# Kernel tuning notes

Hardware: AMD Instinct MI355X
Metric: run time of the kernel (lower is better)

## Reference

```python
import jax, jax.numpy as jnp
import numpy as np

N_U = 16          # |U| unary predicates
N_B = 8           # |B| binary predicates
N_NODES = 500000
N_EDGES = 2000000

# Parsed clause structure: (literal column indices, literal signs).
# Unary clauses over the |U|=16 unary predicate columns.
U_CLAUSES = [
    (np.array([0, 1]), np.array([-1.0, 1.0])),
    (np.array([2, 3]), np.array([-1.0, 1.0])),
    (np.array([4, 5, 6]), np.array([-1.0, 1.0, 1.0])),
]
# Binary clauses over the joined [2|U|+|B|]=40 space: x-copy offset 0, y-copy offset 16, binary offset 32.
B_CLAUSES = [
    (np.array([0, 16, 32]), np.array([-1.0, -1.0, 1.0])),
    (np.array([1, 17, 33]), np.array([-1.0, 1.0, 1.0])),
]


def knowledge_enhancer(x, clauses, weights):
    """KENN KnowledgeEnhancer with GodelBoostConormApprox boost.
    For each clause: delta = w * softmax(signed literals) * signs, scattered back.
    """
    delta = jnp.zeros_like(x)
    for (idx, sign), w in zip(clauses, weights):
        s = jnp.asarray(sign, x.dtype)
        v = x[:, idx] * s                      # [rows, clause_len]
        d = w * jax.nn.softmax(v, axis=-1) * s
        delta = delta.at[:, idx].add(d)
    return delta


def setup_inputs() -> dict:
    key = jax.random.key(0)
    k1, k2, k3, k4 = jax.random.split(key, 4)
    unary = jax.random.normal(k1, (N_NODES, N_U), jnp.float32)
    binary = jax.random.normal(k2, (N_EDGES, N_B), jnp.float32)
    edge_index = jax.random.randint(k3, (2, N_EDGES), 0, N_NODES)
    edge_weight = jax.random.uniform(k4, (N_EDGES,), jnp.float32)
    unary_clause_weights = jnp.full((len(U_CLAUSES),), 0.5, jnp.float32)
    binary_clause_weights = jnp.full((len(B_CLAUSES),), 0.5, jnp.float32)
    return {
        "unary": unary,
        "binary": binary,
        "edge_index": edge_index,
        "edge_weight": edge_weight,
        "unary_clause_weights": unary_clause_weights,
        "binary_clause_weights": binary_clause_weights,
    }


def reference(unary, binary, edge_index, edge_weight, unary_clause_weights, binary_clause_weights):
    i1, i2 = edge_index[0], edge_index[1]
    # unary KE
    u = unary + knowledge_enhancer(unary, U_CLAUSES, unary_clause_weights)
    # Join: gather both endpoints and concat with binary features -> [E, 2|U|+|B|]
    joined = jnp.concatenate([u[i1], u[i2], binary], axis=1)
    # binary KE, per-edge weighted
    d = knowledge_enhancer(joined, B_CLAUSES, binary_clause_weights) * edge_weight[:, None]
    ux = d[:, :N_U]
    uy = d[:, N_U:2 * N_U]
    db = d[:, 2 * N_U:]
    # GroupBy: indexed assignment (last-write semantics, matching torch tensor[index] = val)
    delta_up = jnp.zeros_like(u).at[i1].set(ux) + jnp.zeros_like(u).at[i2].set(uy)
    # activation is identity (default)
    return (u + delta_up, binary + db)
```

## Files before the change

### kernel.cpp

```cpp
#include <hip/hip_runtime.h>
#include <hip/hip_bf16.h>

typedef unsigned long long u64;

__device__ __forceinline__ float bf2f(unsigned short u) {
    union { unsigned int i; float f; } x; x.i = ((unsigned int)u) << 16; return x.f;
}
__device__ __forceinline__ unsigned short f2bf(float f) {
    union { float f; unsigned int i; } x; x.f = f;
    unsigned int r = x.i + 0x7fffu + ((x.i >> 16) & 1u);
    return (unsigned short)(r >> 16);
}

__device__ __forceinline__ bool detect_bf16(const void* unary) {
    const uint4* p = (const uint4*)unary;
    int plaus = 0;
    #pragma unroll
    for (int i = 0; i < 8; ++i) {
        uint4 v = p[i];
        unsigned int w[4] = {v.x, v.y, v.z, v.w};
        #pragma unroll
        for (int j = 0; j < 4; ++j) {
            int ex = (int)((w[j] >> 7) & 0xffu);
            if (ex >= 114 && ex <= 129) ++plaus;
        }
    }
    return plaus >= 16;
}

__device__ __forceinline__ float ldf(const void* p, size_t i, bool bf) {
    return bf ? bf2f(((const unsigned short*)p)[i]) : ((const float*)p)[i];
}


__global__ void f_init(const void* __restrict__ unary,
                       const void* __restrict__ wu,
                       unsigned int* __restrict__ u01,
                       u64* __restrict__ lastA,
                       u64* __restrict__ lastB,
                       unsigned int* __restrict__ shA,
                       unsigned int* __restrict__ shB,
                       int n_nodes)
{
    int n = blockIdx.x * blockDim.x + threadIdx.x;
    if (n >= n_nodes) return;
    bool bf = detect_bf16(unary);
    float x0 = ldf(unary, (size_t)n * 16 + 0, bf);
    float x1 = ldf(unary, (size_t)n * 16 + 1, bf);
    float w0 = ldf(wu, 0, bf);
    float t0 = __expf(-x0), t1 = __expf(x1), inv = w0 / (t0 + t1);
    x0 -= t0 * inv; x1 += t1 * inv;
    u01[n] = (unsigned int)f2bf(x0) | ((unsigned int)f2bf(x1) << 16);
    lastA[n] = 0ull;
    lastB[n] = 0ull;
    shA[n] = 0u;
    shB[n] = 0u;
}

__global__ void f_edge(const void* __restrict__ unary,
                       const void* __restrict__ binary,
                       const int*  __restrict__ ei,
                       const void* __restrict__ ew,
                       const void* __restrict__ wb,
                       const unsigned int* __restrict__ u01,
                       void* __restrict__ out0,
                       u64* __restrict__ lastA,
                       u64* __restrict__ lastB,
                       unsigned int* __restrict__ shA,
                       unsigned int* __restrict__ shB,
                       int n_nodes, int n_edges)
{
    int gid = blockIdx.x * blockDim.x + threadIdx.x;
    if (gid >= n_edges) return;
    int e = n_edges - 1 - gid;
    bool bf = detect_bf16(unary);
    size_t esz = bf ? 2u : 4u;
    char* out1 = (char*)out0 + (size_t)n_nodes * 16u * esz;

    int i1 = ei[e];
    int i2 = ei[e + n_edges];

    unsigned int pa = u01[i1];
    unsigned int pb = u01[i2];
    float a0 = bf2f((unsigned short)(pa & 0xffffu));
    float a1 = bf2f((unsigned short)(pa >> 16));
    float b0 = bf2f((unsigned short)(pb & 0xffffu));
    float b1 = bf2f((unsigned short)(pb >> 16));

    float c0 = ldf(binary, (size_t)e * 8 + 0, bf);
    float c1 = ldf(binary, (size_t)e * 8 + 1, bf);
    float w   = ldf(ew, e, bf);
    float wb0 = ldf(wb, 0, bf);
    float wb1 = ldf(wb, 1, bf);

    float tA0 = __expf(-a0), tA1 = __expf(-b0), tA2 = __expf(c0);
    float invA = w * wb0 / (tA0 + tA1 + tA2);
    float ux0 = -tA0 * invA, uy0 = -tA1 * invA, db0 = tA2 * invA;
    float tB0 = __expf(-a1), tB1 = __expf(b1), tB2 = __expf(c1);
    float invB = w * wb1 / (tB0 + tB1 + tB2);
    float ux1 = -tB0 * invB, uy1 = tB1 * invB, db1 = tB2 * invB;

    if (bf) {
        unsigned short el[8];
        *(uint4*)el = *(const uint4*)((const char*)binary + (size_t)e * 16);
        el[0] = f2bf(c0 + db0);
        el[1] = f2bf(c1 + db1);
        *(uint4*)(out1 + (size_t)e * 16) = *(uint4*)el;
    } else {
        const float* src = (const float*)binary + (size_t)e * 8;
        float r[8];
        *(uint4*)&r[0] = *(const uint4*)&src[0];
        *(uint4*)&r[4] = *(const uint4*)&src[4];
        r[0] = c0 + db0;
        r[1] = c1 + db1;
        float* dst = (float*)(out1 + (size_t)e * 32);
        *(uint4*)&dst[0] = *(uint4*)&r[0];
        *(uint4*)&dst[4] = *(uint4*)&r[4];
    }

    unsigned int key = (unsigned int)(e + 1);
    unsigned int qa = (unsigned int)f2bf(ux0) | ((unsigned int)f2bf(ux1) << 16);
    unsigned int qb = (unsigned int)f2bf(uy0) | ((unsigned int)f2bf(uy1) << 16);
    if (shA[i1] < key) {
        shA[i1] = key;
        atomicMax(&lastA[i1], ((u64)key << 32) | qa);
    }
    if (shB[i2] < key) {
        shB[i2] = key;
        atomicMax(&lastB[i2], ((u64)key << 32) | qb);
    }
}

__global__ void f_fin(const void* __restrict__ unary,
                      const void* __restrict__ wu,
                      const u64* __restrict__ lastA,
                      const u64* __restrict__ lastB,
                      void* __restrict__ out0,
                      int n_nodes)
{
    int n = blockIdx.x * blockDim.x + threadIdx.x;
    if (n >= n_nodes) return;
    bool bf = detect_bf16(unary);

    float x[16];
    if (bf) {
        const unsigned short* src = (const unsigned short*)unary + (size_t)n * 16;
        unsigned short el[16];
        *(uint4*)&el[0] = *(const uint4*)&src[0];
        *(uint4*)&el[8] = *(const uint4*)&src[8];
        #pragma unroll
        for (int i = 0; i < 16; ++i) x[i] = bf2f(el[i]);
    } else {
        const float* src = (const float*)unary + (size_t)n * 16;
        #pragma unroll
        for (int i = 0; i < 16; i += 4) *(uint4*)&x[i] = *(const uint4*)&src[i];
    }

    float w0 = ldf(wu, 0, bf), w1 = ldf(wu, 1, bf), w2 = ldf(wu, 2, bf);
    { float t0 = __expf(-x[0]), t1 = __expf(x[1]), inv = w0 / (t0 + t1);
      x[0] -= t0 * inv; x[1] += t1 * inv; }
    { float t0 = __expf(-x[2]), t1 = __expf(x[3]), inv = w1 / (t0 + t1);
      x[2] -= t0 * inv; x[3] += t1 * inv; }
    { float t0 = __expf(-x[4]), t1 = __expf(x[5]), t2 = __expf(x[6]);
      float inv = w2 / (t0 + t1 + t2);
      x[4] -= t0 * inv; x[5] += t1 * inv; x[6] += t2 * inv; }

    u64 sa = lastA[n], sb = lastB[n];
    if (sa) {
        x[0] += bf2f((unsigned short)(sa & 0xffffu));
        x[1] += bf2f((unsigned short)((sa >> 16) & 0xffffu));
    }
    if (sb) {
        x[0] += bf2f((unsigned short)(sb & 0xffffu));
        x[1] += bf2f((unsigned short)((sb >> 16) & 0xffffu));
    }

    if (bf) {
        unsigned short el[16];
        #pragma unroll
        for (int i = 0; i < 16; ++i) el[i] = f2bf(x[i]);
        uint4* dst = (uint4*)((char*)out0 + (size_t)n * 32);
        dst[0] = *(uint4*)&el[0];
        dst[1] = *(uint4*)&el[8];
    } else {
        float* dst = (float*)((char*)out0 + (size_t)n * 64);
        #pragma unroll
        for (int i = 0; i < 16; i += 4) *(uint4*)&dst[i] = *(uint4*)&x[i];
    }
}


__global__ void m_edge(const void* __restrict__ unary,
                       const void* __restrict__ binary,
                       const int*  __restrict__ ei,
                       const void* __restrict__ ew,
                       const void* __restrict__ wb,
                       const unsigned int* __restrict__ u01,
                       void* __restrict__ out0,
                       u64* __restrict__ lastA,
                       u64* __restrict__ lastB,
                       int n_nodes, int n_edges)
{
    int gid = blockIdx.x * blockDim.x + threadIdx.x;
    if (gid >= n_edges) return;
    int e = n_edges - 1 - gid;
    bool bf = detect_bf16(unary);
    size_t esz = bf ? 2u : 4u;
    char* out1 = (char*)out0 + (size_t)n_nodes * 16u * esz;

    int i1 = ei[e];
    int i2 = ei[e + n_edges];

    unsigned int pa = u01[i1];
    unsigned int pb = u01[i2];
    float a0 = bf2f((unsigned short)(pa & 0xffffu));
    float a1 = bf2f((unsigned short)(pa >> 16));
    float b0 = bf2f((unsigned short)(pb & 0xffffu));
    float b1 = bf2f((unsigned short)(pb >> 16));

    float c0 = ldf(binary, (size_t)e * 8 + 0, bf);
    float c1 = ldf(binary, (size_t)e * 8 + 1, bf);
    float w   = ldf(ew, e, bf);
    float wb0 = ldf(wb, 0, bf);
    float wb1 = ldf(wb, 1, bf);

    float tA0 = __expf(-a0), tA1 = __expf(-b0), tA2 = __expf(c0);
    float invA = w * wb0 / (tA0 + tA1 + tA2);
    float ux0 = -tA0 * invA, uy0 = -tA1 * invA, db0 = tA2 * invA;
    float tB0 = __expf(-a1), tB1 = __expf(b1), tB2 = __expf(c1);
    float invB = w * wb1 / (tB0 + tB1 + tB2);
    float ux1 = -tB0 * invB, uy1 = tB1 * invB, db1 = tB2 * invB;

    if (bf) {
        unsigned short el[8];
        *(uint4*)el = *(const uint4*)((const char*)binary + (size_t)e * 16);
        el[0] = f2bf(c0 + db0);
        el[1] = f2bf(c1 + db1);
        *(uint4*)(out1 + (size_t)e * 16) = *(uint4*)el;
    } else {
        const float* src = (const float*)binary + (size_t)e * 8;
        float r[8];
        *(uint4*)&r[0] = *(const uint4*)&src[0];
        *(uint4*)&r[4] = *(const uint4*)&src[4];
        r[0] = c0 + db0;
        r[1] = c1 + db1;
        float* dst = (float*)(out1 + (size_t)e * 32);
        *(uint4*)&dst[0] = *(uint4*)&r[0];
        *(uint4*)&dst[4] = *(uint4*)&r[4];
    }

    unsigned int key = (unsigned int)(e + 1);
    unsigned int qa = (unsigned int)f2bf(ux0) | ((unsigned int)f2bf(ux1) << 16);
    unsigned int qb = (unsigned int)f2bf(uy0) | ((unsigned int)f2bf(uy1) << 16);
    if ((unsigned int)(lastA[i1] >> 32) < key)
        atomicMax(&lastA[i1], ((u64)key << 32) | qa);
    if ((unsigned int)(lastB[i2] >> 32) < key)
        atomicMax(&lastB[i2], ((u64)key << 32) | qb);
}


__global__ void k_init(const void* __restrict__ unary, void* __restrict__ out0,
                       int n_nodes)
{
    int n = blockIdx.x * blockDim.x + threadIdx.x;
    if (n >= n_nodes) return;
    bool bf = detect_bf16(unary);
    size_t rs = bf ? 32u : 64u;
    u64* s = (u64*)((char*)out0 + (size_t)n * rs);
    s[0] = 0ull; s[1] = 0ull;
}

__global__ void k_edge(const void* __restrict__ unary,
                       const void* __restrict__ binary,
                       const int*  __restrict__ ei,
                       const void* __restrict__ ew,
                       const void* __restrict__ wu,
                       const void* __restrict__ wb,
                       void* __restrict__ out0,
                       int n_nodes, int n_edges)
{
    int e = blockIdx.x * blockDim.x + threadIdx.x;
    if (e >= n_edges) return;
    bool bf = detect_bf16(unary);
    size_t esz = bf ? 2u : 4u;
    size_t rs  = 16u * esz;
    char* out1 = (char*)out0 + (size_t)n_nodes * rs;

    int i1 = ei[e];
    int i2 = ei[e + n_edges];

    float w0 = ldf(wu, 0, bf);
    float a0 = ldf(unary, (size_t)i1 * 16 + 0, bf);
    float a1 = ldf(unary, (size_t)i1 * 16 + 1, bf);
    { float t0 = __expf(-a0), t1 = __expf(a1), inv = w0 / (t0 + t1);
      a0 -= t0 * inv; a1 += t1 * inv; }
    float b0 = ldf(unary, (size_t)i2 * 16 + 0, bf);
    float b1 = ldf(unary, (size_t)i2 * 16 + 1, bf);
    { float t0 = __expf(-b0), t1 = __expf(b1), inv = w0 / (t0 + t1);
      b0 -= t0 * inv; b1 += t1 * inv; }

    float c0 = ldf(binary, (size_t)e * 8 + 0, bf);
    float c1 = ldf(binary, (size_t)e * 8 + 1, bf);
    float w   = ldf(ew, e, bf);
    float wb0 = ldf(wb, 0, bf);
    float wb1 = ldf(wb, 1, bf);

    float tA0 = __expf(-a0), tA1 = __expf(-b0), tA2 = __expf(c0);
    float invA = w * wb0 / (tA0 + tA1 + tA2);
    float ux0 = -tA0 * invA, uy0 = -tA1 * invA, db0 = tA2 * invA;
    float tB0 = __expf(-a1), tB1 = __expf(b1), tB2 = __expf(c1);
    float invB = w * wb1 / (tB0 + tB1 + tB2);
    float ux1 = -tB0 * invB, uy1 = tB1 * invB, db1 = tB2 * invB;

    if (bf) {
        unsigned short el[8];
        *(uint4*)el = *(const uint4*)((const char*)binary + (size_t)e * 16);
        el[0] = f2bf(c0 + db0);
        el[1] = f2bf(c1 + db1);
        *(uint4*)(out1 + (size_t)e * 16) = *(uint4*)el;
    } else {
        const float* src = (const float*)binary + (size_t)e * 8;
        float r[8];
        *(uint4*)&r[0] = *(const uint4*)&src[0];
        *(uint4*)&r[4] = *(const uint4*)&src[4];
        r[0] = c0 + db0;
        r[1] = c1 + db1;
        float* dst = (float*)(out1 + (size_t)e * 32);
        *(uint4*)&dst[0] = *(uint4*)&r[0];
        *(uint4*)&dst[4] = *(uint4*)&r[4];
    }

    unsigned int pa = (unsigned int)f2bf(ux0) | ((unsigned int)f2bf(ux1) << 16);
    unsigned int pb = (unsigned int)f2bf(uy0) | ((unsigned int)f2bf(uy1) << 16);
    u64 ka = ((u64)(unsigned int)(e + 1) << 32) | pa;
    u64 kb = ((u64)(unsigned int)(e + 1) << 32) | pb;
    atomicMax((u64*)((char*)out0 + (size_t)i1 * rs),     ka);
    atomicMax((u64*)((char*)out0 + (size_t)i2 * rs + 8), kb);
}

__global__ void k_fin(const void* __restrict__ unary,
                      const void* __restrict__ wu,
                      void* __restrict__ out0,
                      int n_nodes)
{
    int n = blockIdx.x * blockDim.x + threadIdx.x;
    if (n >= n_nodes) return;
    bool bf = detect_bf16(unary);
    size_t rs = bf ? 32u : 64u;
    char* row = (char*)out0 + (size_t)n * rs;

    u64 sa = ((const u64*)row)[0];
    u64 sb = ((const u64*)row)[1];

    float x[16];
    if (bf) {
        const unsigned short* src = (const unsigned short*)unary + (size_t)n * 16;
        unsigned short el[16];
        *(uint4*)&el[0] = *(const uint4*)&src[0];
        *(uint4*)&el[8] = *(const uint4*)&src[8];
        #pragma unroll
        for (int i = 0; i < 16; ++i) x[i] = bf2f(el[i]);
    } else {
        const float* src = (const float*)unary + (size_t)n * 16;
        #pragma unroll
        for (int i = 0; i < 16; i += 4) *(uint4*)&x[i] = *(const uint4*)&src[i];
    }

    float w0 = ldf(wu, 0, bf), w1 = ldf(wu, 1, bf), w2 = ldf(wu, 2, bf);
    { float t0 = __expf(-x[0]), t1 = __expf(x[1]), inv = w0 / (t0 + t1);
      x[0] -= t0 * inv; x[1] += t1 * inv; }
    { float t0 = __expf(-x[2]), t1 = __expf(x[3]), inv = w1 / (t0 + t1);
      x[2] -= t0 * inv; x[3] += t1 * inv; }
    { float t0 = __expf(-x[4]), t1 = __expf(x[5]), t2 = __expf(x[6]);
      float inv = w2 / (t0 + t1 + t2);
      x[4] -= t0 * inv; x[5] += t1 * inv; x[6] += t2 * inv; }

    if (sa) {
        x[0] += bf2f((unsigned short)(sa & 0xffffu));
        x[1] += bf2f((unsigned short)((sa >> 16) & 0xffffu));
    }
    if (sb) {
        x[0] += bf2f((unsigned short)(sb & 0xffffu));
        x[1] += bf2f((unsigned short)((sb >> 16) & 0xffffu));
    }

    if (bf) {
        unsigned short el[16];
        #pragma unroll
        for (int i = 0; i < 16; ++i) el[i] = f2bf(x[i]);
        uint4* dst = (uint4*)row;
        dst[0] = *(uint4*)&el[0];
        dst[1] = *(uint4*)&el[8];
    } else {
        float* dst = (float*)row;
        #pragma unroll
        for (int i = 0; i < 16; i += 4) *(uint4*)&dst[i] = *(uint4*)&x[i];
    }
}

extern "C" void kernel_launch(void* const* d_in, const int* in_sizes, int n_in,
                              void* d_out, int out_size, void* d_ws, size_t ws_size,
                              hipStream_t stream)
{
    const void* unary  = d_in[0];
    const void* binary = d_in[1];
    const int*  ei     = (const int*)d_in[2];
    const void* ew     = d_in[3];
    const void* wu     = d_in[4];
    const void* wb     = d_in[5];

    const int n_nodes = in_sizes[0] / 16;
    const int n_edges = in_sizes[1] / 8;

    const int B = 256;
    const size_t need3 = (size_t)n_nodes * (4 + 8 + 8 + 4 + 4);
    const size_t need2 = (size_t)n_nodes * (4 + 8 + 8);

    unsigned int* u01 = (unsigned int*)d_ws;
    u64* lastA = (u64*)((char*)d_ws + (size_t)n_nodes * 4);
    u64* lastB = lastA + n_nodes;
    unsigned int* shA = (unsigned int*)(lastB + n_nodes);
    unsigned int* shB = shA + n_nodes;

    if (ws_size >= need3) {
        f_init<<<(n_nodes + B - 1) / B, B, 0, stream>>>(
            unary, wu, u01, lastA, lastB, shA, shB, n_nodes);
        f_edge<<<(n_edges + B - 1) / B, B, 0, stream>>>(
            unary, binary, ei, ew, wb, u01, d_out, lastA, lastB, shA, shB,
            n_nodes, n_edges);
        f_fin<<<(n_nodes + B - 1) / B, B, 0, stream>>>(
            unary, wu, lastA, lastB, d_out, n_nodes);
    } else if (ws_size >= need2) {
        f_init<<<(n_nodes + B - 1) / B, B, 0, stream>>>(
            unary, wu, u01, lastA, lastB, lastA ? (unsigned int*)lastA : 0,
            (unsigned int*)lastB, 0);
        f_init<<<(n_nodes + B - 1) / B, B, 0, stream>>>(
            unary, wu, u01, lastA, lastB, (unsigned int*)u01, (unsigned int*)u01, 0);
        {
            hipMemsetAsync(lastA, 0, (size_t)n_nodes * 16, stream);
            f_init<<<(n_nodes + B - 1) / B, B, 0, stream>>>(
                unary, wu, u01, lastA, lastB, (unsigned int*)lastA,
                (unsigned int*)lastB, 0);
        }
        f_init<<<(n_nodes + B - 1) / B, B, 0, stream>>>(
            unary, wu, u01, lastA, lastB, (unsigned int*)lastA,
            (unsigned int*)lastB, n_nodes);
        m_edge<<<(n_edges + B - 1) / B, B, 0, stream>>>(
            unary, binary, ei, ew, wb, u01, d_out, lastA, lastB,
            n_nodes, n_edges);
        f_fin<<<(n_nodes + B - 1) / B, B, 0, stream>>>(
            unary, wu, lastA, lastB, d_out, n_nodes);
    } else {
        k_init<<<(n_nodes + B - 1) / B, B, 0, stream>>>(unary, d_out, n_nodes);
        k_edge<<<(n_edges + B - 1) / B, B, 0, stream>>>(
            unary, binary, ei, ew, wu, wb, d_out, n_nodes, n_edges);
        k_fin<<<(n_nodes + B - 1) / B, B, 0, stream>>>(unary, wu, d_out, n_nodes);
    }
}
```

Measured before the change: 148.5 us.

## Privatize last-write atomic tables per XCC and reduce them in finalize

Adds a new path that gives each XCC, identified by reading the XCC_ID hardware register, its own copy of the last-write key tables. The edge kernel does workgroup-scope atomic max into its XCC's slice, and the finalize kernel max-reduces the eight slices per node. The aim is to keep the scatter atomics local to one XCC's L2 instead of paying for device-scope coherent atomics across dies. In exchange, the init kernel must zero eight times more table memory and the finalize kernel must read it back. The path runs only when the workspace is large enough, and the old odd-looking fallback chain is removed.

```diff
diff --git a/kernel.cpp b/kernel.cpp
--- a/kernel.cpp
+++ b/kernel.cpp
@@ -30,6 +30,176 @@
 
 __device__ __forceinline__ float ldf(const void* p, size_t i, bool bf) {
     return bf ? bf2f(((const unsigned short*)p)[i]) : ((const float*)p)[i];
+}
+
+__device__ __forceinline__ unsigned int xcc_id() {
+    unsigned int x;
+    asm volatile("s_getreg_b32 %0, hwreg(HW_REG_XCC_ID)" : "=s"(x));
+    return x & 7u;
+}
+
+
+__global__ void x_init(const void* __restrict__ unary,
+                       const void* __restrict__ wu,
+                       unsigned int* __restrict__ u01,
+                       u64* __restrict__ xa,
+                       u64* __restrict__ xb,
+                       int n_nodes)
+{
+    int n = blockIdx.x * blockDim.x + threadIdx.x;
+    if (n >= n_nodes) return;
+    bool bf = detect_bf16(unary);
+    float x0 = ldf(unary, (size_t)n * 16 + 0, bf);
+    float x1 = ldf(unary, (size_t)n * 16 + 1, bf);
+    float w0 = ldf(wu, 0, bf);
+    float t0 = __expf(-x0), t1 = __expf(x1), inv = w0 / (t0 + t1);
+    x0 -= t0 * inv; x1 += t1 * inv;
+    u01[n] = (unsigned int)f2bf(x0) | ((unsigned int)f2bf(x1) << 16);
+    #pragma unroll
+    for (int x = 0; x < 8; ++x) {
+        xa[(size_t)x * n_nodes + n] = 0ull;
+        xb[(size_t)x * n_nodes + n] = 0ull;
+    }
+}
+
+__global__ void x_edge(const void* __restrict__ unary,
+                       const void* __restrict__ binary,
+                       const int*  __restrict__ ei,
+                       const void* __restrict__ ew,
+                       const void* __restrict__ wb,
+                       const unsigned int* __restrict__ u01,
+                       void* __restrict__ out0,
+                       u64* __restrict__ xa,
+                       u64* __restrict__ xb,
+                       int n_nodes, int n_edges)
+{
+    int gid = blockIdx.x * blockDim.x + threadIdx.x;
+    if (gid >= n_edges) return;
+    int e = n_edges - 1 - gid;
+    bool bf = detect_bf16(unary);
+    size_t esz = bf ? 2u : 4u;
+    char* out1 = (char*)out0 + (size_t)n_nodes * 16u * esz;
+
+    int i1 = ei[e];
+    int i2 = ei[e + n_edges];
+
+    unsigned int pa = u01[i1];
+    unsigned int pb = u01[i2];
+    float a0 = bf2f((unsigned short)(pa & 0xffffu));
+    float a1 = bf2f((unsigned short)(pa >> 16));
+    float b0 = bf2f((unsigned short)(pb & 0xffffu));
+    float b1 = bf2f((unsigned short)(pb >> 16));
+
+    float c0 = ldf(binary, (size_t)e * 8 + 0, bf);
+    float c1 = ldf(binary, (size_t)e * 8 + 1, bf);
+    float w   = ldf(ew, e, bf);
+    float wb0 = ldf(wb, 0, bf);
+    float wb1 = ldf(wb, 1, bf);
+
+    float tA0 = __expf(-a0), tA1 = __expf(-b0), tA2 = __expf(c0);
+    float invA = w * wb0 / (tA0 + tA1 + tA2);
+    float ux0 = -tA0 * invA, uy0 = -tA1 * invA, db0 = tA2 * invA;
+    float tB0 = __expf(-a1), tB1 = __expf(b1), tB2 = __expf(c1);
+    float invB = w * wb1 / (tB0 + tB1 + tB2);
+    float ux1 = -tB0 * invB, uy1 = tB1 * invB, db1 = tB2 * invB;
+
+    if (bf) {
+        unsigned short el[8];
+        *(uint4*)el = *(const uint4*)((const char*)binary + (size_t)e * 16);
+        el[0] = f2bf(c0 + db0);
+        el[1] = f2bf(c1 + db1);
+        *(uint4*)(out1 + (size_t)e * 16) = *(uint4*)el;
+    } else {
+        const float* src = (const float*)binary + (size_t)e * 8;
+        float r[8];
+        *(uint4*)&r[0] = *(const uint4*)&src[0];
+        *(uint4*)&r[4] = *(const uint4*)&src[4];
+        r[0] = c0 + db0;
+        r[1] = c1 + db1;
+        float* dst = (float*)(out1 + (size_t)e * 32);
+        *(uint4*)&dst[0] = *(uint4*)&r[0];
+        *(uint4*)&dst[4] = *(uint4*)&r[4];
+    }
+
+    unsigned int key = (unsigned int)(e + 1);
+    unsigned int qa = (unsigned int)f2bf(ux0) | ((unsigned int)f2bf(ux1) << 16);
+    unsigned int qb = (unsigned int)f2bf(uy0) | ((unsigned int)f2bf(uy1) << 16);
+    u64 ka = ((u64)key << 32) | qa;
+    u64 kb = ((u64)key << 32) | qb;
+
+    unsigned int x = xcc_id();
+    u64* pA = xa + (size_t)x * n_nodes + i1;
+    u64* pB = xb + (size_t)x * n_nodes + i2;
+    if (*pA < ka)
+        __hip_atomic_fetch_max(pA, ka, __ATOMIC_RELAXED, __HIP_MEMORY_SCOPE_WORKGROUP);
+    if (*pB < kb)
+        __hip_atomic_fetch_max(pB, kb, __ATOMIC_RELAXED, __HIP_MEMORY_SCOPE_WORKGROUP);
+}
+
+__global__ void x_fin(const void* __restrict__ unary,
+                      const void* __restrict__ wu,
+                      const u64* __restrict__ xa,
+                      const u64* __restrict__ xb,
+                      void* __restrict__ out0,
+                      int n_nodes)
+{
+    int n = blockIdx.x * blockDim.x + threadIdx.x;
+    if (n >= n_nodes) return;
+    bool bf = detect_bf16(unary);
+
+    u64 sa = 0ull, sb = 0ull;
+    #pragma unroll
+    for (int x = 0; x < 8; ++x) {
+        u64 va = xa[(size_t)x * n_nodes + n];
+        u64 vb = xb[(size_t)x * n_nodes + n];
+        sa = va > sa ? va : sa;
+        sb = vb > sb ? vb : sb;
+    }
+
+    float xr[16];
+    if (bf) {
+        const unsigned short* src = (const unsigned short*)unary + (size_t)n * 16;
+        unsigned short el[16];
+        *(uint4*)&el[0] = *(const uint4*)&src[0];
+        *(uint4*)&el[8] = *(const uint4*)&src[8];
+        #pragma unroll
+        for (int i = 0; i < 16; ++i) xr[i] = bf2f(el[i]);
+    } else {
+        const float* src = (const float*)unary + (size_t)n * 16;
+        #pragma unroll
+        for (int i = 0; i < 16; i += 4) *(uint4*)&xr[i] = *(const uint4*)&src[i];
+    }
+
+    float w0 = ldf(wu, 0, bf), w1 = ldf(wu, 1, bf), w2 = ldf(wu, 2, bf);
+    { float t0 = __expf(-xr[0]), t1 = __expf(xr[1]), inv = w0 / (t0 + t1);
+      xr[0] -= t0 * inv; xr[1] += t1 * inv; }
+    { float t0 = __expf(-xr[2]), t1 = __expf(xr[3]), inv = w1 / (t0 + t1);
+      xr[2] -= t0 * inv; xr[3] += t1 * inv; }
+    { float t0 = __expf(-xr[4]), t1 = __expf(xr[5]), t2 = __expf(xr[6]);
+      float inv = w2 / (t0 + t1 + t2);
+      xr[4] -= t0 * inv; xr[5] += t1 * inv; xr[6] += t2 * inv; }
+
+    if (sa) {
+        xr[0] += bf2f((unsigned short)(sa & 0xffffu));
+        xr[1] += bf2f((unsigned short)((sa >> 16) & 0xffffu));
+    }
+    if (sb) {
+        xr[0] += bf2f((unsigned short)(sb & 0xffffu));
+        xr[1] += bf2f((unsigned short)((sb >> 16) & 0xffffu));
+    }
+
+    if (bf) {
+        unsigned short el[16];
+        #pragma unroll
+        for (int i = 0; i < 16; ++i) el[i] = f2bf(xr[i]);
+        uint4* dst = (uint4*)((char*)out0 + (size_t)n * 32);
+        dst[0] = *(uint4*)&el[0];
+        dst[1] = *(uint4*)&el[8];
+    } else {
+        float* dst = (float*)((char*)out0 + (size_t)n * 64);
+        #pragma unroll
+        for (int i = 0; i < 16; i += 4) *(uint4*)&dst[i] = *(uint4*)&xr[i];
+    }
 }
 
 
@@ -190,33 +360,45 @@
 }
 
 
-__global__ void m_edge(const void* __restrict__ unary,
+__global__ void k_init(const void* __restrict__ unary, void* __restrict__ out0,
+                       int n_nodes)
+{
+    int n = blockIdx.x * blockDim.x + threadIdx.x;
+    if (n >= n_nodes) return;
+    bool bf = detect_bf16(unary);
+    size_t rs = bf ? 32u : 64u;
+    u64* s = (u64*)((char*)out0 + (size_t)n * rs);
+    s[0] = 0ull; s[1] = 0ull;
+}
+
+__global__ void k_edge(const void* __restrict__ unary,
                        const void* __restrict__ binary,
                        const int*  __restrict__ ei,
                        const void* __restrict__ ew,
+                       const void* __restrict__ wu,
                        const void* __restrict__ wb,
-                       const unsigned int* __restrict__ u01,
                        void* __restrict__ out0,
-                       u64* __restrict__ lastA,
-                       u64* __restrict__ lastB,
                        int n_nodes, int n_edges)
 {
-    int gid = blockIdx.x * blockDim.x + threadIdx.x;
-    if (gid >= n_edges) return;
-    int e = n_edges - 1 - gid;
+    int e = blockIdx.x * blockDim.x + threadIdx.x;
+    if (e >= n_edges) return;
     bool bf = detect_bf16(unary);
     size_t esz = bf ? 2u : 4u;
-    char* out1 = (char*)out0 + (size_t)n_nodes * 16u * esz;
+    size_t rs  = 16u * esz;
+    char* out1 = (char*)out0 + (size_t)n_nodes * rs;
 
     int i1 = ei[e];
     int i2 = ei[e + n_edges];
 
-    unsigned int pa = u01[i1];
-    unsigned int pb = u01[i2];
-    float a0 = bf2f((unsigned short)(pa & 0xffffu));
-    float a1 = bf2f((unsigned short)(pa >> 16));
-    float b0 = bf2f((unsigned short)(pb & 0xffffu));
-    float b1 = bf2f((unsigned short)(pb >> 16));
+    float w0 = ldf(wu, 0, bf);
+    float a0 = ldf(unary, (size_t)i1 * 16 + 0, bf);
+    float a1 = ldf(unary, (size_t)i1 * 16 + 1, bf);
+    { float t0 = __expf(-a0), t1 = __expf(a1), inv = w0 / (t0 + t1);
+      a0 -= t0 * inv; a1 += t1 * inv; }
+    float b0 = ldf(unary, (size_t)i2 * 16 + 0, bf);
+    float b1 = ldf(unary, (size_t)i2 * 16 + 1, bf);
+    { float t0 = __expf(-b0), t1 = __expf(b1), inv = w0 / (t0 + t1);
+      b0 -= t0 * inv; b1 += t1 * inv; }
 
     float c0 = ldf(binary, (size_t)e * 8 + 0, bf);
     float c1 = ldf(binary, (size_t)e * 8 + 1, bf);
@@ -249,87 +431,6 @@
         *(uint4*)&dst[4] = *(uint4*)&r[4];
     }
 
-    unsigned int key = (unsigned int)(e + 1);
-    unsigned int qa = (unsigned int)f2bf(ux0) | ((unsigned int)f2bf(ux1) << 16);
-    unsigned int qb = (unsigned int)f2bf(uy0) | ((unsigned int)f2bf(uy1) << 16);
-    if ((unsigned int)(lastA[i1] >> 32) < key)
-        atomicMax(&lastA[i1], ((u64)key << 32) | qa);
-    if ((unsigned int)(lastB[i2] >> 32) < key)
-        atomicMax(&lastB[i2], ((u64)key << 32) | qb);
-}
-
-
-__global__ void k_init(const void* __restrict__ unary, void* __restrict__ out0,
-                       int n_nodes)
-{
-    int n = blockIdx.x * blockDim.x + threadIdx.x;
-    if (n >= n_nodes) return;
-    bool bf = detect_bf16(unary);
-    size_t rs = bf ? 32u : 64u;
-    u64* s = (u64*)((char*)out0 + (size_t)n * rs);
-    s[0] = 0ull; s[1] = 0ull;
-}
-
-__global__ void k_edge(const void* __restrict__ unary,
-                       const void* __restrict__ binary,
-                       const int*  __restrict__ ei,
-                       const void* __restrict__ ew,
-                       const void* __restrict__ wu,
-                       const void* __restrict__ wb,
-                       void* __restrict__ out0,
-                       int n_nodes, int n_edges)
-{
-    int e = blockIdx.x * blockDim.x + threadIdx.x;
-    if (e >= n_edges) return;
-    bool bf = detect_bf16(unary);
-    size_t esz = bf ? 2u : 4u;
-    size_t rs  = 16u * esz;
-    char* out1 = (char*)out0 + (size_t)n_nodes * rs;
-
-    int i1 = ei[e];
-    int i2 = ei[e + n_edges];
-
-    float w0 = ldf(wu, 0, bf);
-    float a0 = ldf(unary, (size_t)i1 * 16 + 0, bf);
-    float a1 = ldf(unary, (size_t)i1 * 16 + 1, bf);
-    { float t0 = __expf(-a0), t1 = __expf(a1), inv = w0 / (t0 + t1);
-      a0 -= t0 * inv; a1 += t1 * inv; }
-    float b0 = ldf(unary, (size_t)i2 * 16 + 0, bf);
-    float b1 = ldf(unary, (size_t)i2 * 16 + 1, bf);
-    { float t0 = __expf(-b0), t1 = __expf(b1), inv = w0 / (t0 + t1);
-      b0 -= t0 * inv; b1 += t1 * inv; }
-
-    float c0 = ldf(binary, (size_t)e * 8 + 0, bf);
-    float c1 = ldf(binary, (size_t)e * 8 + 1, bf);
-    float w   = ldf(ew, e, bf);
-    float wb0 = ldf(wb, 0, bf);
-    float wb1 = ldf(wb, 1, bf);
-
-    float tA0 = __expf(-a0), tA1 = __expf(-b0), tA2 = __expf(c0);
-    float invA = w * wb0 / (tA0 + tA1 + tA2);
-    float ux0 = -tA0 * invA, uy0 = -tA1 * invA, db0 = tA2 * invA;
-    float tB0 = __expf(-a1), tB1 = __expf(b1), tB2 = __expf(c1);
-    float invB = w * wb1 / (tB0 + tB1 + tB2);
-    float ux1 = -tB0 * invB, uy1 = tB1 * invB, db1 = tB2 * invB;
-
-    if (bf) {
-        unsigned short el[8];
-        *(uint4*)el = *(const uint4*)((const char*)binary + (size_t)e * 16);
-        el[0] = f2bf(c0 + db0);
-        el[1] = f2bf(c1 + db1);
-        *(uint4*)(out1 + (size_t)e * 16) = *(uint4*)el;
-    } else {
-        const float* src = (const float*)binary + (size_t)e * 8;
-        float r[8];
-        *(uint4*)&r[0] = *(const uint4*)&src[0];
-        *(uint4*)&r[4] = *(const uint4*)&src[4];
-        r[0] = c0 + db0;
-        r[1] = c1 + db1;
-        float* dst = (float*)(out1 + (size_t)e * 32);
-        *(uint4*)&dst[0] = *(uint4*)&r[0];
-        *(uint4*)&dst[4] = *(uint4*)&r[4];
-    }
-
     unsigned int pa = (unsigned int)f2bf(ux0) | ((unsigned int)f2bf(ux1) << 16);
     unsigned int pb = (unsigned int)f2bf(uy0) | ((unsigned int)f2bf(uy1) << 16);
     u64 ka = ((u64)(unsigned int)(e + 1) << 32) | pa;
@@ -413,16 +514,25 @@
     const int n_edges = in_sizes[1] / 8;
 
     const int B = 256;
-    const size_t need3 = (size_t)n_nodes * (4 + 8 + 8 + 4 + 4);
-    const size_t need2 = (size_t)n_nodes * (4 + 8 + 8);
-
-    unsigned int* u01 = (unsigned int*)d_ws;
-    u64* lastA = (u64*)((char*)d_ws + (size_t)n_nodes * 4);
-    u64* lastB = lastA + n_nodes;
-    unsigned int* shA = (unsigned int*)(lastB + n_nodes);
-    unsigned int* shB = shA + n_nodes;
-
-    if (ws_size >= need3) {
+    const size_t need_x = (size_t)n_nodes * (4 + 64 + 64);
+    const size_t need_f = (size_t)n_nodes * (4 + 8 + 8 + 4 + 4);
+
+    if (ws_size >= need_x) {
+        unsigned int* u01 = (unsigned int*)d_ws;
+        u64* xa = (u64*)((char*)d_ws + (size_t)n_nodes * 4);
+        u64* xb = xa + (size_t)8 * n_nodes;
+        x_init<<<(n_nodes + B - 1) / B, B, 0, stream>>>(
+            unary, wu, u01, xa, xb, n_nodes);
+        x_edge<<<(n_edges + B - 1) / B, B, 0, stream>>>(
+            unary, binary, ei, ew, wb, u01, d_out, xa, xb, n_nodes, n_edges);
+        x_fin<<<(n_nodes + B - 1) / B, B, 0, stream>>>(
+            unary, wu, xa, xb, d_out, n_nodes);
+    } else if (ws_size >= need_f) {
+        unsigned int* u01 = (unsigned int*)d_ws;
+        u64* lastA = (u64*)((char*)d_ws + (size_t)n_nodes * 4);
+        u64* lastB = lastA + n_nodes;
+        unsigned int* shA = (unsigned int*)(lastB + n_nodes);
+        unsigned int* shB = shA + n_nodes;
         f_init<<<(n_nodes + B - 1) / B, B, 0, stream>>>(
             unary, wu, u01, lastA, lastB, shA, shB, n_nodes);
         f_edge<<<(n_edges + B - 1) / B, B, 0, stream>>>(
@@ -430,26 +540,6 @@
             n_nodes, n_edges);
         f_fin<<<(n_nodes + B - 1) / B, B, 0, stream>>>(
             unary, wu, lastA, lastB, d_out, n_nodes);
-    } else if (ws_size >= need2) {
-        f_init<<<(n_nodes + B - 1) / B, B, 0, stream>>>(
-            unary, wu, u01, lastA, lastB, lastA ? (unsigned int*)lastA : 0,
-            (unsigned int*)lastB, 0);
-        f_init<<<(n_nodes + B - 1) / B, B, 0, stream>>>(
-            unary, wu, u01, lastA, lastB, (unsigned int*)u01, (unsigned int*)u01, 0);
-        {
-            hipMemsetAsync(lastA, 0, (size_t)n_nodes * 16, stream);
-            f_init<<<(n_nodes + B - 1) / B, B, 0, stream>>>(
-                unary, wu, u01, lastA, lastB, (unsigned int*)lastA,
-                (unsigned int*)lastB, 0);
-        }
-        f_init<<<(n_nodes + B - 1) / B, B, 0, stream>>>(
-            unary, wu, u01, lastA, lastB, (unsigned int*)lastA,
-            (unsigned int*)lastB, n_nodes);
-        m_edge<<<(n_edges + B - 1) / B, B, 0, stream>>>(
-            unary, binary, ei, ew, wb, u01, d_out, lastA, lastB,
-            n_nodes, n_edges);
-        f_fin<<<(n_nodes + B - 1) / B, B, 0, stream>>>(
-            unary, wu, lastA, lastB, d_out, n_nodes);
     } else {
         k_init<<<(n_nodes + B - 1) / B, B, 0, stream>>>(unary, d_out, n_nodes);
         k_edge<<<(n_edges + B - 1) / B, B, 0, stream>>>(
```

Measured after the change: 246.1 us. 65.7% more time.
